# Kernel optimization log

Hardware: AMD Instinct MI355X
Metric: run time of the kernel (lower is better)

## Reference

```python
import jax, jax.numpy as jnp
import numpy as np


def conv2d(x, w, b, pad=0):
    y = jax.lax.conv_general_dilated(x, w, (1, 1), [(pad, pad), (pad, pad)],
                                     dimension_numbers=('NCHW', 'OIHW', 'NCHW'))
    return y + b[None, :, None, None]


def leaky(x):
    return jnp.where(x >= 0, x, 0.1 * x)


def adaptive_pool3(x):
    # exact AdaptiveAvgPool2d((3,3)) when H,W divisible by 3
    B, C, H, W = x.shape
    return x.reshape(B, C, 3, H // 3, 3, W // 3).mean(axis=(3, 5))


def psf2otf(ker, H, W):
    # circularly shift PSF so its centre is at (0,0), then FFT (DWDN convention)
    B, C, kh, kw = ker.shape
    c = kh // 2 + 1
    psf = jnp.zeros((B, C, H, W), ker.dtype)
    psf = psf.at[:, :, :c, :c].set(ker[:, :, c - 1:, c - 1:])
    psf = psf.at[:, :, :c, -(c - 1):].set(ker[:, :, c - 1:, :c - 1])
    psf = psf.at[:, :, -(c - 1):, :c].set(ker[:, :, :c - 1, c - 1:])
    psf = psf.at[:, :, -(c - 1):, -(c - 1):].set(ker[:, :, :c - 1, :c - 1])
    return jnp.fft.fft2(psf)


def setup_inputs() -> dict:
    key = jax.random.key(0)
    ks = jax.random.split(key, 16)
    B, NF, C, H = 8, 64, 16, 246
    x = jax.random.normal(ks[0], (B, NF, H, H), jnp.float32)
    kernel = jax.random.uniform(ks[1], (B, 1, 21, 21), jnp.float32)
    kernel = kernel / kernel.sum(axis=(2, 3), keepdims=True)  # normalized blur PSF
    def w(k, shape):
        fan_in = shape[1] * shape[2] * shape[3]
        return jax.random.normal(k, shape, jnp.float32) / np.sqrt(fan_in)
    return {
        'x': x, 'kernel': kernel,
        'w_red': w(ks[2], (C, NF, 1, 1)), 'b_red': jnp.zeros((C,), jnp.float32),
        'w_g1': w(ks[3], (C, C, 3, 3)), 'b_g1': jnp.zeros((C,), jnp.float32),
        'w_g2': w(ks[4], (C, C, 3, 3)), 'b_g2': jnp.zeros((C,), jnp.float32),
        'w_g3': w(ks[5], (C, C, 3, 3)), 'b_g3': jnp.zeros((C,), jnp.float32),
        'w_g4': w(ks[6], (C, C, 1, 1)), 'b_g4': jnp.zeros((C,), jnp.float32),
        'w_exp': w(ks[7], (NF, C, 1, 1)), 'b_exp': jnp.zeros((NF,), jnp.float32),
    }


def reference(x, kernel, w_red, b_red, w_g1, b_g1, w_g2, b_g2, w_g3, b_g3,
              w_g4, b_g4, w_exp, b_exp):
    cls_feats = conv2d(x, w_red, b_red)                      # [B,C,H,W]
    h = leaky(conv2d(cls_feats, w_g1, b_g1))                 # valid 3x3 convs
    h = leaky(conv2d(h, w_g2, b_g2))
    h = conv2d(h, w_g3, b_g3)
    h = adaptive_pool3(h)                                    # [B,C,3,3]
    kernel_P = jnp.exp(conv2d(h, w_g4, b_g4))
    kernel_P = kernel_P - kernel_P.mean(axis=(2, 3), keepdims=True)

    ks_ = kernel.shape[-1]
    fp = jnp.pad(cls_feats, ((0, 0), (0, 0), (ks_, ks_), (ks_, ks_)), mode='edge')
    Hp, Wp = fp.shape[2], fp.shape[3]
    # batched Wiener deconvolution over all channels at once (replaces per-channel loop)
    Kf = psf2otf(kernel, Hp, Wp)                             # [B,1,Hp,Wp] complex
    Pf = psf2otf(kernel_P, Hp, Wp)                           # [B,C,Hp,Wp] complex
    denom = Kf.real ** 2 + Kf.imag ** 2 + Pf.real ** 2 + Pf.imag ** 2
    inv_ker = jnp.conj(Kf) / denom                           # conj(K)/(|K|^2+|P|^2)
    deblur = jnp.fft.ifft2(inv_ker * jnp.fft.fft2(fp)).real
    clear = deblur[:, :, ks_:-ks_, ks_:-ks_]
    return conv2d(clear, w_exp, b_exp)
```

## Files before the change

### kernel.cpp

```cpp
#include <hip/hip_runtime.h>
#include <hip/hip_bf16.h>

__device__ inline float2 cadd(float2 a, float2 b){ return make_float2(a.x+b.x, a.y+b.y); }
__device__ inline float2 csub(float2 a, float2 b){ return make_float2(a.x-b.x, a.y-b.y); }
__device__ inline float2 cmul(float2 a, float2 b){
    return make_float2(fmaf(a.x,b.x,-a.y*b.y), fmaf(a.x,b.y,a.y*b.x));
}

#define NPIX 60516
#define NFFT 288
#define NFFT2 82944

template<bool INV>
__device__ inline void bf4(float2 a0, float2 a1, float2 a2, float2 a3,
                           float2& b0, float2& b1, float2& b2, float2& b3) {
    float2 t0=cadd(a0,a2), t1=csub(a0,a2), t2=cadd(a1,a3), t3=csub(a1,a3);
    b0=cadd(t0,t2); b2=csub(t0,t2);
    if (!INV) { b1=make_float2(t1.x+t3.y, t1.y-t3.x); b3=make_float2(t1.x-t3.y, t1.y+t3.x); }
    else      { b1=make_float2(t1.x-t3.y, t1.y+t3.x); b3=make_float2(t1.x+t3.y, t1.y-t3.x); }
}
template<bool INV>
__device__ inline void bf3(float2 a0, float2 a1, float2 a2,
                           float2& b0, float2& b1, float2& b2) {
    const float d = INV ? 0.8660254037844386f : -0.8660254037844386f;
    float2 tt=cadd(a1,a2), u=csub(a1,a2);
    b0=cadd(a0,tt);
    b1=make_float2(a0.x-0.5f*tt.x - d*u.y, a0.y-0.5f*tt.y + d*u.x);
    b2=make_float2(a0.x-0.5f*tt.x + d*u.y, a0.y-0.5f*tt.y - d*u.x);
}

template<bool INV>
__device__ inline void fft288_row(float2*& X, float2*& Y, int lane, const float2* __restrict__ tw) {
    auto TW = [&](int k) { float2 v = tw[k]; if (INV) v.y = -v.y; return v; };
    for (int p = lane; p < 72; p += 64) {
        float2 b0,b1,b2,b3;
        bf4<INV>(X[p], X[p+72], X[p+144], X[p+216], b0,b1,b2,b3);
        Y[4*p]=b0; Y[4*p+1]=cmul(b1,TW(p)); Y[4*p+2]=cmul(b2,TW(2*p)); Y[4*p+3]=cmul(b3,TW(3*p));
    }
    __syncthreads(); { float2* t=X; X=Y; Y=t; }
    for (int it = lane; it < 72; it += 64) {
        int p = it>>2, q = it&3, i0 = q+4*p;
        float2 b0,b1,b2,b3;
        bf4<INV>(X[i0], X[i0+72], X[i0+144], X[i0+216], b0,b1,b2,b3);
        int o = q+16*p;
        Y[o]=b0; Y[o+4]=cmul(b1,TW(4*p)); Y[o+8]=cmul(b2,TW(8*p)); Y[o+12]=cmul(b3,TW(12*p));
    }
    __syncthreads(); { float2* t=X; X=Y; Y=t; }
    for (int it = lane; it < 144; it += 64) {
        int p = it>>4, q = it&15, i0 = q+16*p;
        float2 a0=X[i0], a1=X[i0+144];
        int o = q+32*p;
        Y[o]=cadd(a0,a1); Y[o+16]=cmul(csub(a0,a1),TW(16*p));
    }
    __syncthreads(); { float2* t=X; X=Y; Y=t; }
    for (int it = lane; it < 96; it += 64) {
        int p = it>>5, q = it&31, i0 = q+32*p;
        float2 b0,b1,b2;
        bf3<INV>(X[i0], X[i0+96], X[i0+192], b0,b1,b2);
        int o = q+96*p;
        Y[o]=b0; Y[o+32]=cmul(b1,TW(32*p)); Y[o+64]=cmul(b2,TW(64*p));
    }
    __syncthreads(); { float2* t=X; X=Y; Y=t; }
    for (int q = lane; q < 96; q += 64) {
        float2 b0,b1,b2;
        bf3<INV>(X[q], X[q+96], X[q+192], b0,b1,b2);
        Y[q]=b0; Y[q+96]=b1; Y[q+192]=b2;
    }
    __syncthreads(); { float2* t=X; X=Y; Y=t; }
}

template<bool INV>
__device__ inline void fft288_s9(float2*& X, float2*& Y, int w, int c, const float2* __restrict__ tw) {
    auto TW = [&](int k) { float2 v = tw[k]; if (INV) v.y = -v.y; return v; };
    #define SIX(i) ((i)*9 + c)
    for (int p = w; p < 72; p += 32) {
        float2 b0,b1,b2,b3;
        bf4<INV>(X[SIX(p)], X[SIX(p+72)], X[SIX(p+144)], X[SIX(p+216)], b0,b1,b2,b3);
        Y[SIX(4*p)]=b0; Y[SIX(4*p+1)]=cmul(b1,TW(p));
        Y[SIX(4*p+2)]=cmul(b2,TW(2*p)); Y[SIX(4*p+3)]=cmul(b3,TW(3*p));
    }
    __syncthreads(); { float2* t=X; X=Y; Y=t; }
    for (int it = w; it < 72; it += 32) {
        int p = it>>2, q = it&3, i0 = q+4*p;
        float2 b0,b1,b2,b3;
        bf4<INV>(X[SIX(i0)], X[SIX(i0+72)], X[SIX(i0+144)], X[SIX(i0+216)], b0,b1,b2,b3);
        int o = q+16*p;
        Y[SIX(o)]=b0; Y[SIX(o+4)]=cmul(b1,TW(4*p));
        Y[SIX(o+8)]=cmul(b2,TW(8*p)); Y[SIX(o+12)]=cmul(b3,TW(12*p));
    }
    __syncthreads(); { float2* t=X; X=Y; Y=t; }
    for (int it = w; it < 144; it += 32) {
        int p = it>>4, q = it&15, i0 = q+16*p;
        float2 a0=X[SIX(i0)], a1=X[SIX(i0+144)];
        int o = q+32*p;
        Y[SIX(o)]=cadd(a0,a1); Y[SIX(o+16)]=cmul(csub(a0,a1),TW(16*p));
    }
    __syncthreads(); { float2* t=X; X=Y; Y=t; }
    for (int it = w; it < 96; it += 32) {
        int p = it>>5, q = it&31, i0 = q+32*p;
        float2 b0,b1,b2;
        bf3<INV>(X[SIX(i0)], X[SIX(i0+96)], X[SIX(i0+192)], b0,b1,b2);
        int o = q+96*p;
        Y[SIX(o)]=b0; Y[SIX(o+32)]=cmul(b1,TW(32*p)); Y[SIX(o+64)]=cmul(b2,TW(64*p));
    }
    __syncthreads(); { float2* t=X; X=Y; Y=t; }
    for (int q = w; q < 96; q += 32) {
        float2 b0,b1,b2;
        bf3<INV>(X[SIX(q)], X[SIX(q+96)], X[SIX(q+192)], b0,b1,b2);
        Y[SIX(q)]=b0; Y[SIX(q+96)]=b1; Y[SIX(q+192)]=b2;
    }
    __syncthreads(); { float2* t=X; X=Y; Y=t; }
    #undef SIX
}

__global__ void k_tw(float2* tw, float* pooled) {
    int t = threadIdx.x;
    if (t < NFFT) {
        double ang = -2.0 * 3.14159265358979323846 * (double)t / (double)NFFT;
        tw[t] = make_float2((float)cos(ang), (float)sin(ang));
    }
    for (int i = t; i < 1152; i += 320) pooled[i] = 0.f;
}

__global__ __launch_bounds__(256) void k_conv1x1_red(const float* __restrict__ x,
        const float* __restrict__ w, const float* __restrict__ bias, float* __restrict__ out) {
    int idx = blockIdx.x * 256 + threadIdx.x;
    if (idx >= 8 * NPIX) return;
    int b = idx / NPIX, p = idx % NPIX;
    const float* xb = x + (size_t)b * 64 * NPIX + p;
    float acc[16];
    #pragma unroll
    for (int co = 0; co < 16; co++) acc[co] = bias[co];
    for (int ci = 0; ci < 64; ci++) {
        float v = xb[(size_t)ci * NPIX];
        #pragma unroll
        for (int co = 0; co < 16; co++) acc[co] = fmaf(w[co*64+ci], v, acc[co]);
    }
    float* ob = out + (size_t)b * 16 * NPIX + p;
    #pragma unroll
    for (int co = 0; co < 16; co++) ob[(size_t)co*NPIX] = acc[co];
}

template<int HIN, bool LEAKY>
__global__ __launch_bounds__(256) void k_conv3x3(const float* __restrict__ in,
        const float* __restrict__ w, const float* __restrict__ bias, float* __restrict__ out) {
    const int HOUT = HIN - 2;
    const int GX = (HOUT + 3) / 4;
    int idx = blockIdx.x * 256 + threadIdx.x;
    if (idx >= 8 * HOUT * GX) return;
    int b  = idx / (HOUT * GX);
    int r  = idx % (HOUT * GX);
    int oy = r / GX;
    int ox0 = (r % GX) * 4;

    float acc[16][4];
    #pragma unroll
    for (int co = 0; co < 16; co++) {
        float bb = bias[co];
        #pragma unroll
        for (int px = 0; px < 4; px++) acc[co][px] = bb;
    }
    const float* ib = in + (size_t)b * 16 * HIN * HIN + (size_t)oy * HIN;
    for (int ci = 0; ci < 16; ci++) {
        const float* ic = ib + (size_t)ci * HIN * HIN;
        #pragma unroll
        for (int ky = 0; ky < 3; ky++) {
            float in6[6];
            #pragma unroll
            for (int j = 0; j < 6; j++) {
                int xx = ox0 + j;
                if (HOUT % 4 != 0) { if (xx > HIN - 1) xx = HIN - 1; }
                in6[j] = ic[ky * HIN + xx];
            }
            #pragma unroll
            for (int kx = 0; kx < 3; kx++) {
                #pragma unroll
                for (int co = 0; co < 16; co++) {
                    float wv = w[co*144 + ci*9 + ky*3 + kx];
                    #pragma unroll
                    for (int px = 0; px < 4; px++)
                        acc[co][px] = fmaf(wv, in6[px + kx], acc[co][px]);
                }
            }
        }
    }
    float* ob = out + (size_t)b * 16 * HOUT * HOUT + (size_t)oy * HOUT + ox0;
    #pragma unroll
    for (int co = 0; co < 16; co++) {
        #pragma unroll
        for (int px = 0; px < 4; px++) {
            if (HOUT % 4 == 0 || ox0 + px < HOUT) {
                float v = acc[co][px];
                if (LEAKY) v = (v >= 0.f) ? v : 0.1f * v;
                ob[(size_t)co * HOUT * HOUT + px] = v;
            }
        }
    }
}

__global__ __launch_bounds__(256) void k_conv3x3_pool(const float* __restrict__ in,
        const float* __restrict__ w, const float* __restrict__ bias, float* __restrict__ pooled) {
    const int HIN = 242, GX = 60;
    __shared__ float cs[144];
    int t = threadIdx.x;
    int b = blockIdx.x / 57;
    int r = (blockIdx.x % 57) * 256 + t;
    bool valid = r < 14400;
    float partial[16];
    int cell = 0;
    if (valid) {
        int oy = r / GX, ox0 = (r % GX) * 4;
        cell = (oy / 80) * 3 + (ox0 / 80);
        float acc[16][4];
        #pragma unroll
        for (int co = 0; co < 16; co++) {
            float bb = bias[co];
            #pragma unroll
            for (int px = 0; px < 4; px++) acc[co][px] = bb;
        }
        const float* ib = in + (size_t)b * 16 * HIN * HIN + (size_t)oy * HIN;
        for (int ci = 0; ci < 16; ci++) {
            const float* ic = ib + (size_t)ci * HIN * HIN;
            #pragma unroll
            for (int ky = 0; ky < 3; ky++) {
                float in6[6];
                #pragma unroll
                for (int j = 0; j < 6; j++) in6[j] = ic[ky * HIN + ox0 + j];
                #pragma unroll
                for (int kx = 0; kx < 3; kx++) {
                    #pragma unroll
                    for (int co = 0; co < 16; co++) {
                        float wv = w[co*144 + ci*9 + ky*3 + kx];
                        #pragma unroll
                        for (int px = 0; px < 4; px++)
                            acc[co][px] = fmaf(wv, in6[px + kx], acc[co][px]);
                    }
                }
            }
        }
        #pragma unroll
        for (int co = 0; co < 16; co++)
            partial[co] = (acc[co][0] + acc[co][1]) + (acc[co][2] + acc[co][3]);
    }
    if (t < 144) cs[t] = 0.f;
    __syncthreads();
    if (valid) {
        #pragma unroll
        for (int co = 0; co < 16; co++) atomicAdd(&cs[co*9 + cell], partial[co]);
    }
    __syncthreads();
    if (t < 144) atomicAdd(&pooled[b*144 + t], cs[t]);
}

__global__ void k_kernelP(const float* __restrict__ pooled, const float* __restrict__ w,
                          const float* __restrict__ bias, float* __restrict__ out) {
    int b = blockIdx.x / 16, co = blockIdx.x % 16;
    __shared__ float vals[9];
    int t = threadIdx.x;
    if (t < 9) {
        float a = 0.f;
        for (int ci = 0; ci < 16; ci++) a += pooled[(b*16+ci)*9 + t] * w[co*16+ci];
        vals[t] = expf(bias[co] + a * (1.f/6400.f));
    }
    __syncthreads();
    if (t < 9) {
        float m = 0.f;
        #pragma unroll
        for (int i = 0; i < 9; i++) m += vals[i];
        m *= (1.f/9.f);
        out[(b*16+co)*9 + t] = vals[t] - m;
    }
}

__global__ __launch_bounds__(256) void k_psfKT(const float* __restrict__ ker, float2* __restrict__ KfT) {
    int idx = blockIdx.x*256 + threadIdx.x;
    if (idx >= 8*NFFT2) return;
    int pos = idx % NFFT2, b = idx / NFFT2;
    int u = pos / NFFT, v = pos % NFFT;
    int ry = (v < 11) ? v+10 : ((v >= 278) ? v-278 : -1);
    int rx = (u < 11) ? u+10 : ((u >= 278) ? u-278 : -1);
    float val = (ry >= 0 && rx >= 0) ? ker[b*441 + ry*21 + rx] : 0.f;
    KfT[idx] = make_float2(val, 0.f);
}

template<bool INV>
__global__ __launch_bounds__(256) void k_fft_rows(float2* __restrict__ M, const float2* __restrict__ tw) {
    __shared__ float2 A[4][NFFT];
    __shared__ float2 B[4][NFFT];
    int t = threadIdx.x, w = t >> 6, lane = t & 63;
    size_t row = (size_t)blockIdx.x*4 + w;
    float2* X = A[w]; float2* Y = B[w];
    float2* s = M + row*NFFT;
    for (int j = lane; j < NFFT; j += 64) X[j] = s[j];
    __syncthreads();
    fft288_row<INV>(X, Y, lane, tw);
    for (int j = lane; j < NFFT; j += 64) s[j] = X[j];
}

template<bool INV>
__global__ __launch_bounds__(256) void k_fft_cols(float2* __restrict__ M, const float2* __restrict__ tw) {
    __shared__ float2 Abuf[NFFT*9];
    __shared__ float2 Bbuf[NFFT*9];
    int t = threadIdx.x, c = t & 7, w = t >> 3;
    int ch = blockIdx.x / 36, cg = blockIdx.x % 36;
    float2* base = M + (size_t)ch * NFFT2 + cg*8 + c;
    float2* X = Abuf; float2* Y = Bbuf;
    for (int r = w; r < NFFT; r += 32) X[r*9 + c] = base[(size_t)r * NFFT];
    __syncthreads();
    fft288_s9<INV>(X, Y, w, c, tw);
    for (int r = w; r < NFFT; r += 32) base[(size_t)r * NFFT] = X[r*9 + c];
}

__global__ __launch_bounds__(256) void k_fft_rows_pad(const float* __restrict__ cls,
        float2* __restrict__ Z, const float2* __restrict__ tw) {
    __shared__ float2 A[4][NFFT];
    __shared__ float2 B[4][NFFT];
    int t = threadIdx.x, w = t >> 6, lane = t & 63;
    size_t row = (size_t)blockIdx.x*4 + w;
    int pc = (int)(row / NFFT), y = (int)(row % NFFT);
    int iy = min(max(y-21, 0), 245);
    const float* c0 = cls + (size_t)(2*pc)*NPIX + (size_t)iy*246;
    float2* X = A[w]; float2* Y = B[w];
    for (int j = lane; j < NFFT; j += 64) {
        int ix = min(max(j-21, 0), 245);
        X[j] = make_float2(c0[ix], c0[NPIX+ix]);
    }
    __syncthreads();
    fft288_row<false>(X, Y, lane, tw);
    float2* d = Z + row*NFFT;
    for (int j = lane; j < NFFT; j += 64) d[j] = X[j];
}

__global__ __launch_bounds__(256) void k_fft_cols_filter(float2* __restrict__ Z,
        const float2* __restrict__ KfT, const float* __restrict__ kP, const float2* __restrict__ tw) {
    __shared__ float2 Abuf[NFFT*9];
    __shared__ float2 Bbuf[NFFT*9];
    int t = threadIdx.x, c = t & 7, w = t >> 3;
    int ch = blockIdx.x / 36, g = blockIdx.x % 36;
    int colc, pi;
    if (g == 0) {
        colc = (c < 4) ? c : (c == 4 ? 144 : 292 - c);
        pi   = (c == 0 || c == 4) ? c : (c < 4 ? c + 4 : c - 4);
    } else {
        colc = (c < 4) ? (4*g + c) : (288 - 4*g - (c - 4));
        pi   = c ^ 4;
    }
    float2* zb = Z + (size_t)ch * NFFT2 + colc;
    float2* X = Abuf; float2* Y = Bbuf;
    for (int r = w; r < NFFT; r += 32) X[r*9 + c] = zb[(size_t)r * NFFT];
    __syncthreads();
    fft288_s9<false>(X, Y, w, c, tw);
    {
        int b = ch >> 3;
        const float* pA = kP + (size_t)(2*ch)*9;
        const float* pB = pA + 9;
        float2 wx = tw[colc];
        const float2* Kcol = KfT + (size_t)b*NFFT2 + (size_t)colc*NFFT;
        for (int y = w; y < NFFT; y += 32) {
            int my = (y == 0) ? 0 : NFFT - y;
            float2 zk = X[y*9 + c];
            float2 zm = X[my*9 + pi];
            float2 K  = Kcol[y];
            float2 wy = tw[y];
            auto otf3 = [&](const float* p9) {
                float2 R0 = make_float2(p9[1] + (p9[0]+p9[2])*wx.x, (p9[2]-p9[0])*wx.y);
                float2 R1 = make_float2(p9[4] + (p9[3]+p9[5])*wx.x, (p9[5]-p9[3])*wx.y);
                float2 R2 = make_float2(p9[7] + (p9[6]+p9[8])*wx.x, (p9[8]-p9[6])*wx.y);
                float2 P;
                P.x = R1.x + wy.x*(R0.x+R2.x) - wy.y*(R2.y-R0.y);
                P.y = R1.y + wy.x*(R0.y+R2.y) + wy.y*(R2.x-R0.x);
                return P;
            };
            float2 Pa = otf3(pA);
            float2 Pb = otf3(pB);
            float2 A_ = make_float2(0.5f*(zk.x+zm.x),  0.5f*(zk.y-zm.y));
            float2 B_ = make_float2(0.5f*(zk.y+zm.y), -0.5f*(zk.x-zm.x));
            float kk = K.x*K.x + K.y*K.y;
            float ra = 1.0f / (kk + Pa.x*Pa.x + Pa.y*Pa.y);
            float rb = 1.0f / (kk + Pb.x*Pb.x + Pb.y*Pb.y);
            float2 Ha = make_float2(K.x*ra, -K.y*ra);
            float2 Hb = make_float2(K.x*rb, -K.y*rb);
            float2 Fa = cmul(Ha, A_);
            float2 Fb = cmul(Hb, B_);
            Y[y*9 + c] = make_float2(Fa.x - Fb.y, Fa.y + Fb.x);
        }
    }
    __syncthreads();
    { float2* tp = X; X = Y; Y = tp; }
    fft288_s9<true>(X, Y, w, c, tw);
    for (int r = w; r < NFFT; r += 32) zb[(size_t)r * NFFT] = X[r*9 + c];
}

__global__ __launch_bounds__(256) void k_ifft_rows_conv(const float2* __restrict__ Z,
        const float* __restrict__ w_exp, const float* __restrict__ b_exp,
        float* __restrict__ out, const float2* __restrict__ tw) {
    __shared__ float2 Abuf[NFFT*9];
    __shared__ float2 Bbuf[NFFT*9];
    int t = threadIdx.x, c = t & 7, w = t >> 3;
    int b = blockIdx.x / 246;
    int rseq = blockIdx.x % 246;
    int y = rseq + 21;
    const float2* s = Z + (size_t)(b*8 + c) * NFFT2 + (size_t)y * NFFT;
    float2* X = Abuf; float2* Y = Bbuf;
    for (int j = w; j < NFFT; j += 32) X[j*9 + c] = s[j];
    __syncthreads();
    fft288_s9<true>(X, Y, w, c, tw);
    if (t < 246) {
        const float sc = 1.0f / 82944.0f;
        float v[16];
        #pragma unroll
        for (int h = 0; h < 8; h++) {
            float2 z = X[(t + 21)*9 + h];
            v[2*h]   = z.x * sc;
            v[2*h+1] = z.y * sc;
        }
        float* ob = out + (size_t)b * 64 * NPIX + (size_t)rseq * 246 + t;
        #pragma unroll
        for (int co = 0; co < 64; co++) {
            float a = b_exp[co];
            #pragma unroll
            for (int ci = 0; ci < 16; ci++) a = fmaf(w_exp[co*16+ci], v[ci], a);
            ob[(size_t)co * NPIX] = a;
        }
    }
}

extern "C" void kernel_launch(void* const* d_in, const int* in_sizes, int n_in,
                              void* d_out, int out_size, void* d_ws, size_t ws_size,
                              hipStream_t stream) {
    const float* x     = (const float*)d_in[0];
    const float* ker   = (const float*)d_in[1];
    const float* w_red = (const float*)d_in[2];
    const float* b_red = (const float*)d_in[3];
    const float* w_g1  = (const float*)d_in[4];
    const float* b_g1  = (const float*)d_in[5];
    const float* w_g2  = (const float*)d_in[6];
    const float* b_g2  = (const float*)d_in[7];
    const float* w_g3  = (const float*)d_in[8];
    const float* b_g3  = (const float*)d_in[9];
    const float* w_g4  = (const float*)d_in[10];
    const float* b_g4  = (const float*)d_in[11];
    const float* w_exp = (const float*)d_in[12];
    const float* b_exp = (const float*)d_in[13];
    float* out = (float*)d_out;

    char* ws = (char*)d_ws;
    size_t off = 0;
    auto alloc = [&](size_t bytes) -> char* {
        char* p = ws + off; off += (bytes + 255) & ~(size_t)255; return p;
    };
    float*  cls    = (float*) alloc(7746048ull * 4);
    float2* Z      = (float2*)alloc((size_t)64 * NFFT2 * 8);
    float*  hb     = (float*) alloc(7495712ull * 4);
    float2* KfT    = (float2*)alloc((size_t)8 * NFFT2 * 8);
    float*  pooled = (float*) alloc(1152 * 4);
    float*  kP     = (float*) alloc(1152 * 4);
    float2* tw     = (float2*)alloc(288 * 8);
    float*  ha     = (float*)Z;

    k_tw<<<1, 320, 0, stream>>>(tw, pooled);
    k_conv1x1_red<<<1892, 256, 0, stream>>>(x, w_red, b_red, cls);
    k_conv3x3<246, true ><<<466, 256, 0, stream>>>(cls, w_g1, b_g1, ha);
    k_conv3x3<244, true ><<<462, 256, 0, stream>>>(ha,  w_g2, b_g2, hb);
    k_conv3x3_pool<<<456, 256, 0, stream>>>(hb, w_g3, b_g3, pooled);
    k_kernelP<<<128, 64, 0, stream>>>(pooled, w_g4, b_g4, kP);

    k_psfKT<<<2592, 256, 0, stream>>>(ker, KfT);
    k_fft_rows<false><<<576, 256, 0, stream>>>(KfT, tw);
    k_fft_cols<false><<<288, 256, 0, stream>>>(KfT, tw);

    k_fft_rows_pad<<<4608, 256, 0, stream>>>(cls, Z, tw);

    k_fft_cols_filter<<<2304, 256, 0, stream>>>(Z, KfT, kP, tw);

    k_ifft_rows_conv<<<1968, 256, 0, stream>>>(Z, w_exp, b_exp, out, tw);
}
```

Measured before the change: 357.7 us.

## Store separated half-spectrum planes and pad LDS layout to avoid bank conflicts

The row FFT of packed channel pairs is now split right away into two half-spectrum planes per real channel (152 columns), which the column filter kernel and the inverse row pass read and rebuild from. This shrinks the column pass work per channel and drops the mirrored-pair logic, but it doubles the channel count, so column work changes from 64x288 to 128x152 columns. Only rows 21..266 are written back. The LDS index adds one padding slot every four rows (lidx) in place of the stride-9 layout, to reduce bank conflicts. The intermediate buffer is somewhat larger and the inverse pass does extra gathers.

```diff
diff --git a/kernel.cpp b/kernel.cpp
--- a/kernel.cpp
+++ b/kernel.cpp
@@ -10,6 +10,11 @@
 #define NPIX 60516
 #define NFFT 288
 #define NFFT2 82944
+#define XW 152
+#define SPLANE (NFFT*XW)
+
+__device__ inline int lidx(int i, int c){ return i*8 + (i>>2) + c; }
+#define LDSN 2376
 
 template<bool INV>
 __device__ inline void bf4(float2 a0, float2 a1, float2 a2, float2 a3,
@@ -72,45 +77,43 @@
 template<bool INV>
 __device__ inline void fft288_s9(float2*& X, float2*& Y, int w, int c, const float2* __restrict__ tw) {
     auto TW = [&](int k) { float2 v = tw[k]; if (INV) v.y = -v.y; return v; };
-    #define SIX(i) ((i)*9 + c)
     for (int p = w; p < 72; p += 32) {
         float2 b0,b1,b2,b3;
-        bf4<INV>(X[SIX(p)], X[SIX(p+72)], X[SIX(p+144)], X[SIX(p+216)], b0,b1,b2,b3);
-        Y[SIX(4*p)]=b0; Y[SIX(4*p+1)]=cmul(b1,TW(p));
-        Y[SIX(4*p+2)]=cmul(b2,TW(2*p)); Y[SIX(4*p+3)]=cmul(b3,TW(3*p));
+        bf4<INV>(X[lidx(p,c)], X[lidx(p+72,c)], X[lidx(p+144,c)], X[lidx(p+216,c)], b0,b1,b2,b3);
+        Y[lidx(4*p,c)]=b0; Y[lidx(4*p+1,c)]=cmul(b1,TW(p));
+        Y[lidx(4*p+2,c)]=cmul(b2,TW(2*p)); Y[lidx(4*p+3,c)]=cmul(b3,TW(3*p));
     }
     __syncthreads(); { float2* t=X; X=Y; Y=t; }
     for (int it = w; it < 72; it += 32) {
         int p = it>>2, q = it&3, i0 = q+4*p;
         float2 b0,b1,b2,b3;
-        bf4<INV>(X[SIX(i0)], X[SIX(i0+72)], X[SIX(i0+144)], X[SIX(i0+216)], b0,b1,b2,b3);
+        bf4<INV>(X[lidx(i0,c)], X[lidx(i0+72,c)], X[lidx(i0+144,c)], X[lidx(i0+216,c)], b0,b1,b2,b3);
         int o = q+16*p;
-        Y[SIX(o)]=b0; Y[SIX(o+4)]=cmul(b1,TW(4*p));
-        Y[SIX(o+8)]=cmul(b2,TW(8*p)); Y[SIX(o+12)]=cmul(b3,TW(12*p));
+        Y[lidx(o,c)]=b0; Y[lidx(o+4,c)]=cmul(b1,TW(4*p));
+        Y[lidx(o+8,c)]=cmul(b2,TW(8*p)); Y[lidx(o+12,c)]=cmul(b3,TW(12*p));
     }
     __syncthreads(); { float2* t=X; X=Y; Y=t; }
     for (int it = w; it < 144; it += 32) {
         int p = it>>4, q = it&15, i0 = q+16*p;
-        float2 a0=X[SIX(i0)], a1=X[SIX(i0+144)];
+        float2 a0=X[lidx(i0,c)], a1=X[lidx(i0+144,c)];
         int o = q+32*p;
-        Y[SIX(o)]=cadd(a0,a1); Y[SIX(o+16)]=cmul(csub(a0,a1),TW(16*p));
+        Y[lidx(o,c)]=cadd(a0,a1); Y[lidx(o+16,c)]=cmul(csub(a0,a1),TW(16*p));
     }
     __syncthreads(); { float2* t=X; X=Y; Y=t; }
     for (int it = w; it < 96; it += 32) {
         int p = it>>5, q = it&31, i0 = q+32*p;
         float2 b0,b1,b2;
-        bf3<INV>(X[SIX(i0)], X[SIX(i0+96)], X[SIX(i0+192)], b0,b1,b2);
+        bf3<INV>(X[lidx(i0,c)], X[lidx(i0+96,c)], X[lidx(i0+192,c)], b0,b1,b2);
         int o = q+96*p;
-        Y[SIX(o)]=b0; Y[SIX(o+32)]=cmul(b1,TW(32*p)); Y[SIX(o+64)]=cmul(b2,TW(64*p));
+        Y[lidx(o,c)]=b0; Y[lidx(o+32,c)]=cmul(b1,TW(32*p)); Y[lidx(o+64,c)]=cmul(b2,TW(64*p));
     }
     __syncthreads(); { float2* t=X; X=Y; Y=t; }
     for (int q = w; q < 96; q += 32) {
         float2 b0,b1,b2;
-        bf3<INV>(X[SIX(q)], X[SIX(q+96)], X[SIX(q+192)], b0,b1,b2);
-        Y[SIX(q)]=b0; Y[SIX(q+96)]=b1; Y[SIX(q+192)]=b2;
-    }
-    __syncthreads(); { float2* t=X; X=Y; Y=t; }
-    #undef SIX
+        bf3<INV>(X[lidx(q,c)], X[lidx(q+96,c)], X[lidx(q+192,c)], b0,b1,b2);
+        Y[lidx(q,c)]=b0; Y[lidx(q+96,c)]=b1; Y[lidx(q+192,c)]=b2;
+    }
+    __syncthreads(); { float2* t=X; X=Y; Y=t; }
 }
 
 __global__ void k_tw(float2* tw, float* pooled) {
@@ -299,20 +302,20 @@
 
 template<bool INV>
 __global__ __launch_bounds__(256) void k_fft_cols(float2* __restrict__ M, const float2* __restrict__ tw) {
-    __shared__ float2 Abuf[NFFT*9];
-    __shared__ float2 Bbuf[NFFT*9];
+    __shared__ float2 Abuf[LDSN];
+    __shared__ float2 Bbuf[LDSN];
     int t = threadIdx.x, c = t & 7, w = t >> 3;
     int ch = blockIdx.x / 36, cg = blockIdx.x % 36;
     float2* base = M + (size_t)ch * NFFT2 + cg*8 + c;
     float2* X = Abuf; float2* Y = Bbuf;
-    for (int r = w; r < NFFT; r += 32) X[r*9 + c] = base[(size_t)r * NFFT];
+    for (int r = w; r < NFFT; r += 32) X[lidx(r,c)] = base[(size_t)r * NFFT];
     __syncthreads();
     fft288_s9<INV>(X, Y, w, c, tw);
-    for (int r = w; r < NFFT; r += 32) base[(size_t)r * NFFT] = X[r*9 + c];
-}
-
-__global__ __launch_bounds__(256) void k_fft_rows_pad(const float* __restrict__ cls,
-        float2* __restrict__ Z, const float2* __restrict__ tw) {
+    for (int r = w; r < NFFT; r += 32) base[(size_t)r * NFFT] = X[lidx(r,c)];
+}
+
+__global__ __launch_bounds__(256) void k_fft_rows_pad_half(const float* __restrict__ cls,
+        float2* __restrict__ S, const float2* __restrict__ tw) {
     __shared__ float2 A[4][NFFT];
     __shared__ float2 B[4][NFFT];
     int t = threadIdx.x, w = t >> 6, lane = t & 63;
@@ -327,82 +330,86 @@
     }
     __syncthreads();
     fft288_row<false>(X, Y, lane, tw);
-    float2* d = Z + row*NFFT;
-    for (int j = lane; j < NFFT; j += 64) d[j] = X[j];
-}
-
-__global__ __launch_bounds__(256) void k_fft_cols_filter(float2* __restrict__ Z,
+    int chA = (pc >> 3)*16 + (pc & 7)*2;
+    float2* sA = S + (size_t)chA * SPLANE + (size_t)y * XW;
+    float2* sB = sA + SPLANE;
+    for (int x = lane; x < XW; x += 64) {
+        float2 Av = make_float2(0.f, 0.f), Bv = make_float2(0.f, 0.f);
+        if (x <= 144) {
+            int m = (NFFT - x) % NFFT;
+            float2 zk = X[x], zm = X[m];
+            Av = make_float2(0.5f*(zk.x+zm.x),  0.5f*(zk.y-zm.y));
+            Bv = make_float2(0.5f*(zk.y+zm.y), -0.5f*(zk.x-zm.x));
+        }
+        sA[x] = Av; sB[x] = Bv;
+    }
+}
+
+__global__ __launch_bounds__(256) void k_fft_cols_filter(float2* __restrict__ S,
         const float2* __restrict__ KfT, const float* __restrict__ kP, const float2* __restrict__ tw) {
-    __shared__ float2 Abuf[NFFT*9];
-    __shared__ float2 Bbuf[NFFT*9];
+    __shared__ float2 Abuf[LDSN];
+    __shared__ float2 Bbuf[LDSN];
     int t = threadIdx.x, c = t & 7, w = t >> 3;
-    int ch = blockIdx.x / 36, g = blockIdx.x % 36;
-    int colc, pi;
-    if (g == 0) {
-        colc = (c < 4) ? c : (c == 4 ? 144 : 292 - c);
-        pi   = (c == 0 || c == 4) ? c : (c < 4 ? c + 4 : c - 4);
-    } else {
-        colc = (c < 4) ? (4*g + c) : (288 - 4*g - (c - 4));
-        pi   = c ^ 4;
-    }
-    float2* zb = Z + (size_t)ch * NFFT2 + colc;
+    int g = blockIdx.x / 128, ch = blockIdx.x % 128;
+    int xg = g*8 + c;
+    int b = ch >> 4;
+    float2* sb = S + (size_t)ch * SPLANE + xg;
     float2* X = Abuf; float2* Y = Bbuf;
-    for (int r = w; r < NFFT; r += 32) X[r*9 + c] = zb[(size_t)r * NFFT];
+    for (int r = w; r < NFFT; r += 32) X[lidx(r,c)] = sb[(size_t)r * XW];
     __syncthreads();
     fft288_s9<false>(X, Y, w, c, tw);
     {
-        int b = ch >> 3;
-        const float* pA = kP + (size_t)(2*ch)*9;
-        const float* pB = pA + 9;
-        float2 wx = tw[colc];
-        const float2* Kcol = KfT + (size_t)b*NFFT2 + (size_t)colc*NFFT;
+        const float* p9 = kP + ch*9;
+        float2 wx = tw[xg];
+        const float2* Kcol = KfT + (size_t)b*NFFT2 + (size_t)xg*NFFT;
         for (int y = w; y < NFFT; y += 32) {
-            int my = (y == 0) ? 0 : NFFT - y;
-            float2 zk = X[y*9 + c];
-            float2 zm = X[my*9 + pi];
-            float2 K  = Kcol[y];
+            float2 v = X[lidx(y,c)];
+            float2 K = Kcol[y];
             float2 wy = tw[y];
-            auto otf3 = [&](const float* p9) {
-                float2 R0 = make_float2(p9[1] + (p9[0]+p9[2])*wx.x, (p9[2]-p9[0])*wx.y);
-                float2 R1 = make_float2(p9[4] + (p9[3]+p9[5])*wx.x, (p9[5]-p9[3])*wx.y);
-                float2 R2 = make_float2(p9[7] + (p9[6]+p9[8])*wx.x, (p9[8]-p9[6])*wx.y);
-                float2 P;
-                P.x = R1.x + wy.x*(R0.x+R2.x) - wy.y*(R2.y-R0.y);
-                P.y = R1.y + wy.x*(R0.y+R2.y) + wy.y*(R2.x-R0.x);
-                return P;
-            };
-            float2 Pa = otf3(pA);
-            float2 Pb = otf3(pB);
-            float2 A_ = make_float2(0.5f*(zk.x+zm.x),  0.5f*(zk.y-zm.y));
-            float2 B_ = make_float2(0.5f*(zk.y+zm.y), -0.5f*(zk.x-zm.x));
+            float2 R0 = make_float2(p9[1] + (p9[0]+p9[2])*wx.x, (p9[2]-p9[0])*wx.y);
+            float2 R1 = make_float2(p9[4] + (p9[3]+p9[5])*wx.x, (p9[5]-p9[3])*wx.y);
+            float2 R2 = make_float2(p9[7] + (p9[6]+p9[8])*wx.x, (p9[8]-p9[6])*wx.y);
+            float2 P;
+            P.x = R1.x + wy.x*(R0.x+R2.x) - wy.y*(R2.y-R0.y);
+            P.y = R1.y + wy.x*(R0.y+R2.y) + wy.y*(R2.x-R0.x);
             float kk = K.x*K.x + K.y*K.y;
-            float ra = 1.0f / (kk + Pa.x*Pa.x + Pa.y*Pa.y);
-            float rb = 1.0f / (kk + Pb.x*Pb.x + Pb.y*Pb.y);
-            float2 Ha = make_float2(K.x*ra, -K.y*ra);
-            float2 Hb = make_float2(K.x*rb, -K.y*rb);
-            float2 Fa = cmul(Ha, A_);
-            float2 Fb = cmul(Hb, B_);
-            Y[y*9 + c] = make_float2(Fa.x - Fb.y, Fa.y + Fb.x);
+            float rcp = 1.0f / (kk + P.x*P.x + P.y*P.y);
+            float2 H = make_float2(K.x*rcp, -K.y*rcp);
+            Y[lidx(y,c)] = cmul(H, v);
         }
     }
     __syncthreads();
     { float2* tp = X; X = Y; Y = tp; }
     fft288_s9<true>(X, Y, w, c, tw);
-    for (int r = w; r < NFFT; r += 32) zb[(size_t)r * NFFT] = X[r*9 + c];
-}
-
-__global__ __launch_bounds__(256) void k_ifft_rows_conv(const float2* __restrict__ Z,
+    for (int r = w; r < NFFT; r += 32)
+        if (r >= 21 && r < 267) sb[(size_t)r * XW] = X[lidx(r,c)];
+}
+
+__global__ __launch_bounds__(256) void k_ifft_rows_conv(const float2* __restrict__ S,
         const float* __restrict__ w_exp, const float* __restrict__ b_exp,
         float* __restrict__ out, const float2* __restrict__ tw) {
-    __shared__ float2 Abuf[NFFT*9];
-    __shared__ float2 Bbuf[NFFT*9];
+    __shared__ float2 Abuf[LDSN];
+    __shared__ float2 Bbuf[LDSN];
     int t = threadIdx.x, c = t & 7, w = t >> 3;
     int b = blockIdx.x / 246;
     int rseq = blockIdx.x % 246;
     int y = rseq + 21;
-    const float2* s = Z + (size_t)(b*8 + c) * NFFT2 + (size_t)y * NFFT;
+    int chA = b*16 + 2*c;
+    const float2* sA = S + (size_t)chA * SPLANE + (size_t)y * XW;
+    const float2* sB = sA + SPLANE;
     float2* X = Abuf; float2* Y = Bbuf;
-    for (int j = w; j < NFFT; j += 32) X[j*9 + c] = s[j];
+    for (int j = w; j < NFFT; j += 32) {
+        float2 z;
+        if (j <= 144) {
+            float2 a = sA[j], bb = sB[j];
+            z = make_float2(a.x - bb.y, a.y + bb.x);
+        } else {
+            int m = NFFT - j;
+            float2 a = sA[m], bb = sB[m];
+            z = make_float2(a.x + bb.y, bb.x - a.y);
+        }
+        X[lidx(j,c)] = z;
+    }
     __syncthreads();
     fft288_s9<true>(X, Y, w, c, tw);
     if (t < 246) {
@@ -410,7 +417,7 @@
         float v[16];
         #pragma unroll
         for (int h = 0; h < 8; h++) {
-            float2 z = X[(t + 21)*9 + h];
+            float2 z = X[lidx(t + 21, h)];
             v[2*h]   = z.x * sc;
             v[2*h+1] = z.y * sc;
         }
@@ -450,13 +457,13 @@
         char* p = ws + off; off += (bytes + 255) & ~(size_t)255; return p;
     };
     float*  cls    = (float*) alloc(7746048ull * 4);
-    float2* Z      = (float2*)alloc((size_t)64 * NFFT2 * 8);
+    float2* S      = (float2*)alloc((size_t)128 * SPLANE * 8);
     float*  hb     = (float*) alloc(7495712ull * 4);
     float2* KfT    = (float2*)alloc((size_t)8 * NFFT2 * 8);
     float*  pooled = (float*) alloc(1152 * 4);
     float*  kP     = (float*) alloc(1152 * 4);
     float2* tw     = (float2*)alloc(288 * 8);
-    float*  ha     = (float*)Z;
+    float*  ha     = (float*)S;
 
     k_tw<<<1, 320, 0, stream>>>(tw, pooled);
     k_conv1x1_red<<<1892, 256, 0, stream>>>(x, w_red, b_red, cls);
@@ -469,9 +476,9 @@
     k_fft_rows<false><<<576, 256, 0, stream>>>(KfT, tw);
     k_fft_cols<false><<<288, 256, 0, stream>>>(KfT, tw);
 
-    k_fft_rows_pad<<<4608, 256, 0, stream>>>(cls, Z, tw);
-
-    k_fft_cols_filter<<<2304, 256, 0, stream>>>(Z, KfT, kP, tw);
-
-    k_ifft_rows_conv<<<1968, 256, 0, stream>>>(Z, w_exp, b_exp, out, tw);
-}
+    k_fft_rows_pad_half<<<4608, 256, 0, stream>>>(cls, S, tw);
+
+    k_fft_cols_filter<<<19*128, 256, 0, stream>>>(S, KfT, kP, tw);
+
+    k_ifft_rows_conv<<<1968, 256, 0, stream>>>(S, w_exp, b_exp, out, tw);
+}
```

After: 342.6 us. -4.2%, faster.
